# Optimization experiments

Measured on AMD Instinct MI355X. Metric: run time of the kernel, lower is better.

Reference implementation:

```python
import jax, jax.numpy as jnp
import numpy as np

N_NODES = 100000
N_EDGES = 1600000
IN_CH = 128
HID = 128
EMBED = 256
NUM_GRAPHS = 128


def setup_inputs() -> dict:
    key = jax.random.key(0)
    ks = jax.random.split(key, 12)
    x = jax.random.normal(ks[0], (N_NODES, IN_CH), dtype=jnp.float32)
    edge_index = jax.random.randint(ks[1], (2, N_EDGES), 0, N_NODES, dtype=jnp.int64)
    batch = jnp.sort(jax.random.randint(ks[2], (N_NODES,), 0, NUM_GRAPHS, dtype=jnp.int64))
    s = 0.05
    # conv1 MLP: Linear(in_ch,128) -> ReLU -> Linear(128,128)
    W11 = jax.random.normal(ks[3], (IN_CH, HID), dtype=jnp.float32) * s
    b11 = jnp.zeros((HID,), dtype=jnp.float32)
    W12 = jax.random.normal(ks[4], (HID, HID), dtype=jnp.float32) * s
    b12 = jnp.zeros((HID,), dtype=jnp.float32)
    # conv2 MLP: Linear(128,128) -> ReLU -> Linear(128,embed)
    W21 = jax.random.normal(ks[5], (HID, HID), dtype=jnp.float32) * s
    b21 = jnp.zeros((HID,), dtype=jnp.float32)
    W22 = jax.random.normal(ks[6], (HID, EMBED), dtype=jnp.float32) * s
    b22 = jnp.zeros((EMBED,), dtype=jnp.float32)
    gamma = jnp.ones((EMBED,), dtype=jnp.float32)
    beta = jnp.zeros((EMBED,), dtype=jnp.float32)
    return {"x": x, "edge_index": edge_index, "batch": batch,
            "W11": W11, "b11": b11, "W12": W12, "b12": b12,
            "W21": W21, "b21": b21, "W22": W22, "b22": b22,
            "gamma": gamma, "beta": beta}


def _gin_conv(x, src, dst, W_a, b_a, W_b, b_b):
    # GINConv with eps=0: MLP(x + sum_{j in N(i)} x_j)
    msgs = x[src]                                   # [E, d] gather
    agg = jax.ops.segment_sum(msgs, dst, num_segments=N_NODES)  # scatter-add
    h = x + agg
    h = jax.nn.relu(h @ W_a + b_a)
    return h @ W_b + b_b


def reference(x, edge_index, batch, W11, b11, W12, b12, W21, b21, W22, b22, gamma, beta):
    src, dst = edge_index[0], edge_index[1]
    h = jax.nn.relu(_gin_conv(x, src, dst, W11, b11, W12, b12))   # [N, 128]
    h = jax.nn.relu(_gin_conv(h, src, dst, W21, b21, W22, b22))   # [N, 256]
    # global_mean_pool over graphs
    sums = jax.ops.segment_sum(h, batch, num_segments=NUM_GRAPHS)           # [G, 256]
    counts = jax.ops.segment_sum(jnp.ones((N_NODES,), h.dtype), batch, num_segments=NUM_GRAPHS)
    pooled = sums / jnp.maximum(counts, 1.0)[:, None]
    # LayerNorm over last dim (eps=1e-5 as in torch)
    mu = jnp.mean(pooled, axis=-1, keepdims=True)
    var = jnp.var(pooled, axis=-1, keepdims=True)
    out = (pooled - mu) * jax.lax.rsqrt(var + 1e-5) * gamma + beta
    # Dropout in eval mode: identity
    return out
```

## Files before the change

kernel.cpp:

```cpp
#include <hip/hip_runtime.h>

#define GRAPHS 128
#define CHUNKC 4000

typedef _Float16 f16x8 __attribute__((ext_vector_type(8)));
typedef _Float16 f16x4 __attribute__((ext_vector_type(4)));
typedef _Float16 f16x2 __attribute__((ext_vector_type(2)));
typedef float f32x4 __attribute__((ext_vector_type(4)));

__device__ __forceinline__ void fmix_lo(float& a, int w) {
  asm("v_fma_mix_f32 %0, %1, 1.0, %0 op_sel:[0,0,0] op_sel_hi:[1,0,0]" : "+v"(a) : "v"(w));
}
__device__ __forceinline__ void fmix_hi(float& a, int w) {
  asm("v_fma_mix_f32 %0, %1, 1.0, %0 op_sel:[1,0,0] op_sel_hi:[1,0,0]" : "+v"(a) : "v"(w));
}

__global__ void k_prep(const int* __restrict__ dst, int* __restrict__ histG,
                       int e, int NB, int NW,
                       const float* __restrict__ x, _Float16* __restrict__ P0,
                       _Float16* __restrict__ P1, int n,
                       const float* __restrict__ W11, const float* __restrict__ W12,
                       const float* __restrict__ W21, const float* __restrict__ W22,
                       f16x8* __restrict__ f11, f16x8* __restrict__ f12,
                       f16x8* __restrict__ f21, f16x8* __restrict__ f22,
                       float* __restrict__ pool, int cvtb, int wpb, int poolb) {
  __shared__ int h[256];
  int b = blockIdx.x, t = threadIdx.x;
  if (b < NW) {
    h[t] = 0; __syncthreads();
    int lo = b * CHUNKC, hi = min(lo + CHUNKC, e);
    for (int i = lo + t; i < hi; i += 256) atomicAdd(&h[dst[i] >> 9], 1);
    __syncthreads();
    if (t < NB) histG[t * NW + b] = h[t];
    return;
  }
  b -= NW;
  if (b < cvtb) {
    int i = b * 256 + t;
    if (i < n * 32) {
      float4 v = ((const float4*)x)[i];
      f16x4 hh = { (_Float16)v.x, (_Float16)v.y, (_Float16)v.z, (_Float16)v.w };
      ((f16x4*)P0)[i] = hh;
    }
    return;
  }
  b -= cvtb;
  if (b < wpb) {
    int id = b * 256 + t;
    const float* W; f16x8* F; int C, cid, fshift;
    if (id < 2048)       { W = W11; F = f11; C = 128; cid = id;        fshift = 3; }
    else if (id < 4096)  { W = W12; F = f12; C = 128; cid = id - 2048; fshift = 3; }
    else if (id < 6144)  { W = W21; F = f21; C = 128; cid = id - 4096; fshift = 3; }
    else if (id < 10240) { W = W22; F = f22; C = 256; cid = id - 6144; fshift = 4; }
    else return;
    int lane = cid & 63;
    int rest = cid >> 6;
    int fc = rest & ((1 << fshift) - 1);
    int kk = rest >> fshift;
    int cout = fc * 16 + (lane & 15);
    int kb = kk * 32 + (lane >> 4) * 8;
    f16x8 v;
#pragma unroll
    for (int q = 0; q < 8; ++q) v[q] = (_Float16)W[(size_t)(kb + q) * C + cout];
    F[cid] = v;
    return;
  }
  b -= wpb;
  if (b < poolb) {
    int i = b * 256 + t;
    if (i < GRAPHS * 256) pool[i] = 0.f;
    return;
  }
  if (t < 128) P0[(size_t)n * 128 + t] = (_Float16)0.f;
  else P1[(size_t)n * 128 + (t - 128)] = (_Float16)0.f;
}

__global__ void k_scanA(const int* __restrict__ in, int* __restrict__ out,
                        int* __restrict__ bsum, int N) {
  __shared__ int s[256];
  int t = threadIdx.x, b = blockIdx.x;
  int base = b * 1024 + t * 4;
  int v[4]; int tot = 0;
#pragma unroll
  for (int j = 0; j < 4; ++j) { int i = base + j; v[j] = (i < N) ? in[i] : 0; tot += v[j]; }
  s[t] = tot; __syncthreads();
  for (int o = 1; o < 256; o <<= 1) {
    int x = (t >= o) ? s[t - o] : 0;
    __syncthreads(); s[t] += x; __syncthreads();
  }
  int run = s[t] - tot;
#pragma unroll
  for (int j = 0; j < 4; ++j) { int i = base + j; if (i < N) out[i] = run; run += v[j]; }
  if (t == 255) bsum[b] = s[255];
}

__global__ void k_scanB(int* bsum, int nb, const int* __restrict__ batch,
                        int* __restrict__ starts, int n) {
  __shared__ int s[256];
  int t = threadIdx.x;
  int v = (t < nb) ? bsum[t] : 0;
  s[t] = v; __syncthreads();
  for (int o = 1; o < 256; o <<= 1) {
    int x = (t >= o) ? s[t - o] : 0;
    __syncthreads(); s[t] += x; __syncthreads();
  }
  if (t < nb) bsum[t] = s[t] - v;
  if (t <= GRAPHS) {
    int lo = 0, hi = n;
    while (lo < hi) { int mid = (lo + hi) >> 1; if (batch[mid] < t) lo = mid + 1; else hi = mid; }
    starts[t] = lo;
  }
}

__global__ void k_part(const int* __restrict__ src, const int* __restrict__ dst,
                       const int* __restrict__ histG, const int* __restrict__ off,
                       const int* __restrict__ bsum,
                       int* __restrict__ part, int e, int NB, int NW) {
  __shared__ int hist[256], lbA[256], lbB[256], stmp[256];
  __shared__ int els[CHUNKC];
  int t = threadIdx.x, w = blockIdx.x;
  int hv = (t < NB) ? histG[t * NW + w] : 0;
  hist[t] = hv; stmp[t] = hv; __syncthreads();
  for (int o = 1; o < 256; o <<= 1) {
    int x = (t >= o) ? stmp[t - o] : 0;
    __syncthreads(); stmp[t] += x; __syncthreads();
  }
  lbA[t] = stmp[t] - hv; lbB[t] = stmp[t] - hv;
  __syncthreads();
  int lo = w * CHUNKC, hi = min(lo + CHUNKC, e);
  for (int i = lo + t; i < hi; i += 256) {
    int d = dst[i];
    int p = atomicAdd(&lbB[d >> 9], 1);
    els[p] = src[i] | ((d & 511) << 17);
  }
  __syncthreads();
  int ln = t & 63, wv = t >> 6;
  for (int b = wv; b < NB; b += 4) {
    int c = hist[b], lb = lbA[b];
    int idx = b * NW + w;
    long g = off[idx] + bsum[idx >> 10];
    for (int j = ln; j < c; j += 64) part[g + j] = els[lb + j];
  }
}

__global__ void k_csrb(const int* __restrict__ part, const int* __restrict__ off,
                       const int* __restrict__ bsum,
                       int* __restrict__ ptr, int* __restrict__ csr,
                       int e, int NB, int NW, int n) {
  __shared__ int nh[512], ncur[512], stmp[256];
  int t = threadIdx.x, b = blockIdx.x;
  int i0 = b * NW;
  int s0 = off[i0] + bsum[i0 >> 10];
  int e0 = e;
  if (b + 1 < NB) { int i1 = (b + 1) * NW; e0 = off[i1] + bsum[i1 >> 10]; }
  nh[t] = 0; nh[t + 256] = 0; __syncthreads();
  for (int i = s0 + t; i < e0; i += 256) atomicAdd(&nh[((unsigned)part[i]) >> 17], 1);
  __syncthreads();
  int v0 = nh[2 * t], v1 = nh[2 * t + 1];
  int ps = v0 + v1;
  stmp[t] = ps; __syncthreads();
  for (int o = 1; o < 256; o <<= 1) {
    int x = (t >= o) ? stmp[t - o] : 0;
    __syncthreads(); stmp[t] += x; __syncthreads();
  }
  int base = stmp[t] - ps;
  __syncthreads();
  nh[2 * t] = base;   nh[2 * t + 1] = base + v0;
  ncur[2 * t] = base; ncur[2 * t + 1] = base + v0;
  __syncthreads();
#pragma unroll
  for (int q = 0; q < 2; ++q) {
    int vv = t + q * 256;
    int node = (b << 9) + vv;
    if (node <= n) ptr[node] = s0 + nh[vv];
  }
  for (int i = s0 + t; i < e0; i += 256) {
    int u = part[i];
    int p = atomicAdd(&ncur[((unsigned)u) >> 17], 1);
    csr[s0 + p] = u & 0x1FFFF;
  }
}

__global__ void k_agg_h(const _Float16* __restrict__ in, _Float16* __restrict__ out,
                        const int* __restrict__ ptr, const int* __restrict__ csr, int n) {
  int gid = blockIdx.x * 256 + threadIdx.x;
  int node = gid >> 6, lane = gid & 63;
  if (node >= n) return;
  const f16x8* inp = (const f16x8*)in;
  int cb = lane & 15, rg = lane >> 4;
  f16x8 self = inp[(size_t)node * 16 + cb];
  float acc[8];
#pragma unroll
  for (int c = 0; c < 8; ++c) acc[c] = (rg == 0) ? (float)self[c] : 0.f;
  int s = ptr[node], deg = ptr[node + 1] - s;
  union W { f16x8 v; int i[4]; };
  for (int seg = 0; seg < deg; seg += 64) {
    int my = (seg + lane < deg) ? csr[s + seg + lane] : n;
    int segn = min(deg - seg, 64);
    for (int b2 = 0; b2 < segn; b2 += 32) {
      int jj[8]; W w[8];
#pragma unroll
      for (int u = 0; u < 8; ++u) jj[u] = __shfl(my, b2 + u * 4 + rg);
#pragma unroll
      for (int u = 0; u < 8; ++u) w[u].v = inp[(size_t)jj[u] * 16 + cb];
#pragma unroll
      for (int u = 0; u < 8; ++u)
#pragma unroll
        for (int p = 0; p < 4; ++p) {
          fmix_lo(acc[2 * p], w[u].i[p]);
          fmix_hi(acc[2 * p + 1], w[u].i[p]);
        }
    }
  }
#pragma unroll
  for (int c = 0; c < 8; ++c) {
    acc[c] += __shfl_xor(acc[c], 16);
    acc[c] += __shfl_xor(acc[c], 32);
  }
  if (rg == 0) {
    f16x8 r;
#pragma unroll
    for (int c = 0; c < 8; ++c) r[c] = (_Float16)acc[c];
    ((f16x8*)out)[(size_t)node * 16 + cb] = r;
  }
}

__device__ __forceinline__ f16x8 xpose(f32x4 aE, f32x4 aO, int rg) {
  union U2 { _Float16 h[2]; int i; };
  union U8 { int i[4]; f16x8 v; };
  U2 e01, e23, o01, o23;
  e01.h[0] = (_Float16)aE[0]; e01.h[1] = (_Float16)aE[1];
  e23.h[0] = (_Float16)aE[2]; e23.h[1] = (_Float16)aE[3];
  o01.h[0] = (_Float16)aO[0]; o01.h[1] = (_Float16)aO[1];
  o23.h[0] = (_Float16)aO[2]; o23.h[1] = (_Float16)aO[3];
  int e01x1 = __shfl_xor(e01.i, 16), e01x2 = __shfl_xor(e01.i, 32), e01x3 = __shfl_xor(e01.i, 48);
  int e23x1 = __shfl_xor(e23.i, 16), e23x2 = __shfl_xor(e23.i, 32), e23x3 = __shfl_xor(e23.i, 48);
  int o01x1 = __shfl_xor(o01.i, 16), o01x2 = __shfl_xor(o01.i, 32), o01x3 = __shfl_xor(o01.i, 48);
  int o23x1 = __shfl_xor(o23.i, 16), o23x2 = __shfl_xor(o23.i, 32), o23x3 = __shfl_xor(o23.i, 48);
  U8 r;
  r.i[0] = rg == 0 ? e01.i : rg == 1 ? e01x3 : rg == 2 ? o01x2 : o01x1;
  r.i[1] = rg == 0 ? e23.i : rg == 1 ? e23x3 : rg == 2 ? o23x2 : o23x1;
  r.i[2] = rg == 0 ? e01x1 : rg == 1 ? e01x2 : rg == 2 ? o01x3 : o01.i;
  r.i[3] = rg == 0 ? e23x1 : rg == 1 ? e23x2 : rg == 2 ? o23x3 : o23.i;
  return r.v;
}

__launch_bounds__(256, 3)
__global__ void k_mlp128(const _Float16* __restrict__ in, const f16x8* __restrict__ wfA,
                         const float* __restrict__ bA, const f16x8* __restrict__ wfB,
                         const float* __restrict__ bB, _Float16* __restrict__ out, int n) {
  __shared__ f16x8 wf[2048];
  int t = threadIdx.x;
  int r0 = blockIdx.x * 128;
  int lane = t & 63, w = t >> 6;
  int l16 = lane & 15, rg = lane >> 4;
  int rw = w * 32;
  const f16x8* inp = (const f16x8*)in;
#pragma unroll
  for (int i = 0; i < 8; ++i) wf[t + i * 256] = wfA[t + i * 256];
  int ra0 = r0 + rw + l16;      if (ra0 > n) ra0 = n;
  int ra1 = r0 + rw + 16 + l16; if (ra1 > n) ra1 = n;
  f16x8 xf[2][4];
#pragma unroll
  for (int kk = 0; kk < 4; ++kk) {
    xf[0][kk] = inp[(size_t)ra0 * 16 + kk * 4 + rg];
    xf[1][kk] = inp[(size_t)ra1 * 16 + kk * 4 + rg];
  }
  __syncthreads();
  f32x4 acc[2][8];
#pragma unroll
  for (int rs = 0; rs < 2; ++rs)
#pragma unroll
    for (int fc = 0; fc < 8; ++fc) acc[rs][fc] = (f32x4){0.f, 0.f, 0.f, 0.f};
#pragma unroll
  for (int kk = 0; kk < 4; ++kk)
#pragma unroll
    for (int fc = 0; fc < 8; ++fc) {
      f16x8 a = wf[(kk * 8 + fc) * 64 + lane];
      acc[0][fc] = __builtin_amdgcn_mfma_f32_16x16x32_f16(a, xf[0][kk], acc[0][fc], 0, 0, 0);
      acc[1][fc] = __builtin_amdgcn_mfma_f32_16x16x32_f16(a, xf[1][kk], acc[1][fc], 0, 0, 0);
    }
  f16x8 hf[2][4];
#pragma unroll
  for (int fc = 0; fc < 8; ++fc) {
    float4 bv = *(const float4*)(bA + fc * 16 + rg * 4);
#pragma unroll
    for (int rs = 0; rs < 2; ++rs) {
      acc[rs][fc][0] = fmaxf(acc[rs][fc][0] + bv.x, 0.f);
      acc[rs][fc][1] = fmaxf(acc[rs][fc][1] + bv.y, 0.f);
      acc[rs][fc][2] = fmaxf(acc[rs][fc][2] + bv.z, 0.f);
      acc[rs][fc][3] = fmaxf(acc[rs][fc][3] + bv.w, 0.f);
    }
  }
#pragma unroll
  for (int rs = 0; rs < 2; ++rs)
#pragma unroll
    for (int kk = 0; kk < 4; ++kk)
      hf[rs][kk] = xpose(acc[rs][2 * kk], acc[rs][2 * kk + 1], rg);
  __syncthreads();
#pragma unroll
  for (int i = 0; i < 8; ++i) wf[t + i * 256] = wfB[t + i * 256];
  __syncthreads();
#pragma unroll
  for (int rs = 0; rs < 2; ++rs)
#pragma unroll
    for (int fc = 0; fc < 8; ++fc) acc[rs][fc] = (f32x4){0.f, 0.f, 0.f, 0.f};
#pragma unroll
  for (int kk = 0; kk < 4; ++kk)
#pragma unroll
    for (int fc = 0; fc < 8; ++fc) {
      f16x8 b = wf[(kk * 8 + fc) * 64 + lane];
      acc[0][fc] = __builtin_amdgcn_mfma_f32_16x16x32_f16(b, hf[0][kk], acc[0][fc], 0, 0, 0);
      acc[1][fc] = __builtin_amdgcn_mfma_f32_16x16x32_f16(b, hf[1][kk], acc[1][fc], 0, 0, 0);
    }
#pragma unroll
  for (int fc = 0; fc < 8; ++fc) {
    float4 bv = *(const float4*)(bB + fc * 16 + rg * 4);
#pragma unroll
    for (int rs = 0; rs < 2; ++rs) {
      acc[rs][fc][0] = fmaxf(acc[rs][fc][0] + bv.x, 0.f);
      acc[rs][fc][1] = fmaxf(acc[rs][fc][1] + bv.y, 0.f);
      acc[rs][fc][2] = fmaxf(acc[rs][fc][2] + bv.z, 0.f);
      acc[rs][fc][3] = fmaxf(acc[rs][fc][3] + bv.w, 0.f);
    }
  }
  f16x8* outp = (f16x8*)out;
#pragma unroll
  for (int rs = 0; rs < 2; ++rs) {
    int row = r0 + rw + rs * 16 + l16;
#pragma unroll
    for (int kk = 0; kk < 4; ++kk) {
      f16x8 o = xpose(acc[rs][2 * kk], acc[rs][2 * kk + 1], rg);
      if (row < n) outp[(size_t)row * 16 + kk * 4 + rg] = o;
    }
  }
}

__launch_bounds__(256, 3)
__global__ void k_mlp_pool(const _Float16* __restrict__ in, const f16x8* __restrict__ wfA,
                           const float* __restrict__ bA, const f16x8* __restrict__ wfB,
                           const float* __restrict__ bB, const int* __restrict__ batch,
                           float* __restrict__ pool, float* __restrict__ scratch, int n) {
  __shared__ f16x8 wf[2048];
  __shared__ float pool_l[8 * 128 * 4];
  int t = threadIdx.x;
  int h = blockIdx.x & 1;
  int r0 = (blockIdx.x >> 1) * 128;
  int lane = t & 63, w = t >> 6;
  int l16 = lane & 15, rg = lane >> 4;
  int rw = w * 32;
  const f16x8* inp = (const f16x8*)in;
#pragma unroll
  for (int j = 0; j < 16; ++j) pool_l[j * 256 + t] = 0.f;
#pragma unroll
  for (int i = 0; i < 8; ++i) wf[t + i * 256] = wfA[t + i * 256];
  int ra0 = r0 + rw + l16;      if (ra0 > n) ra0 = n;
  int ra1 = r0 + rw + 16 + l16; if (ra1 > n) ra1 = n;
  f16x8 xf[2][4];
#pragma unroll
  for (int kk = 0; kk < 4; ++kk) {
    xf[0][kk] = inp[(size_t)ra0 * 16 + kk * 4 + rg];
    xf[1][kk] = inp[(size_t)ra1 * 16 + kk * 4 + rg];
  }
  int g0 = batch[r0];
  int rloc = rw + rg * 4;
  int g4[2][4];
#pragma unroll
  for (int fr = 0; fr < 2; ++fr)
#pragma unroll
    for (int j = 0; j < 4; ++j) {
      int row = r0 + rloc + fr * 16 + j;
      g4[fr][j] = (row < n) ? batch[row] : -1;
    }
  __syncthreads();
  f32x4 acc[2][8];
#pragma unroll
  for (int rs = 0; rs < 2; ++rs)
#pragma unroll
    for (int fc = 0; fc < 8; ++fc) acc[rs][fc] = (f32x4){0.f, 0.f, 0.f, 0.f};
#pragma unroll
  for (int kk = 0; kk < 4; ++kk)
#pragma unroll
    for (int fc = 0; fc < 8; ++fc) {
      f16x8 a = wf[(kk * 8 + fc) * 64 + lane];
      acc[0][fc] = __builtin_amdgcn_mfma_f32_16x16x32_f16(a, xf[0][kk], acc[0][fc], 0, 0, 0);
      acc[1][fc] = __builtin_amdgcn_mfma_f32_16x16x32_f16(a, xf[1][kk], acc[1][fc], 0, 0, 0);
    }
  f16x8 hf[2][4];
#pragma unroll
  for (int fc = 0; fc < 8; ++fc) {
    float4 bv = *(const float4*)(bA + fc * 16 + rg * 4);
#pragma unroll
    for (int rs = 0; rs < 2; ++rs) {
      acc[rs][fc][0] = fmaxf(acc[rs][fc][0] + bv.x, 0.f);
      acc[rs][fc][1] = fmaxf(acc[rs][fc][1] + bv.y, 0.f);
      acc[rs][fc][2] = fmaxf(acc[rs][fc][2] + bv.z, 0.f);
      acc[rs][fc][3] = fmaxf(acc[rs][fc][3] + bv.w, 0.f);
    }
  }
#pragma unroll
  for (int rs = 0; rs < 2; ++rs)
#pragma unroll
    for (int kk = 0; kk < 4; ++kk)
      hf[rs][kk] = xpose(acc[rs][2 * kk], acc[rs][2 * kk + 1], rg);
  __syncthreads();
#pragma unroll
  for (int i = 0; i < 8; ++i) {
    int id = t + i * 256;
    int lj = id & 63, fcl = (id >> 6) & 7, kk = id >> 9;
    wf[id] = wfB[(kk * 16 + h * 8 + fcl) * 64 + lj];
  }
  __syncthreads();
#pragma unroll
  for (int rs = 0; rs < 2; ++rs)
#pragma unroll
    for (int fc = 0; fc < 8; ++fc) acc[rs][fc] = (f32x4){0.f, 0.f, 0.f, 0.f};
#pragma unroll
  for (int kk = 0; kk < 4; ++kk)
#pragma unroll
    for (int fc = 0; fc < 8; ++fc) {
      f16x8 b = wf[(kk * 8 + fc) * 64 + lane];
      acc[0][fc] = __builtin_amdgcn_mfma_f32_16x16x32_f16(hf[0][kk], b, acc[0][fc], 0, 0, 0);
      acc[1][fc] = __builtin_amdgcn_mfma_f32_16x16x32_f16(hf[1][kk], b, acc[1][fc], 0, 0, 0);
    }
#pragma unroll
  for (int fc = 0; fc < 8; ++fc) {
    int col128 = fc * 16 + l16;
    float bv = bB[h * 128 + col128];
#pragma unroll
    for (int fr = 0; fr < 2; ++fr) {
      f32x4 a = acc[fr][fc];
      float run = fmaxf(a[0] + bv, 0.f);
#pragma unroll
      for (int j = 1; j < 4; ++j) {
        float v = fmaxf(a[j] + bv, 0.f);
        if (g4[fr][j] == g4[fr][j - 1]) run += v;
        else {
          int g = g4[fr][j - 1];
          if (g >= 0) {
            int d = g - g0;
            if (d >= 0 && d < 8) atomicAdd(&pool_l[(d * 128 + col128) * 4 + rg], run);
            else atomicAdd(&pool[g * 256 + h * 128 + col128], run);
          }
          run = v;
        }
      }
      int g = g4[fr][3];
      if (g >= 0) {
        int d = g - g0;
        if (d >= 0 && d < 8) atomicAdd(&pool_l[(d * 128 + col128) * 4 + rg], run);
        else atomicAdd(&pool[g * 256 + h * 128 + col128], run);
      }
    }
  }
  __syncthreads();
  float* sb = scratch + (size_t)blockIdx.x * 1024;
#pragma unroll
  for (int j = 0; j < 4; ++j) {
    int idx = j * 256 + t;
    float4 v4 = *(const float4*)&pool_l[idx * 4];
    sb[idx] = (v4.x + v4.y) + (v4.z + v4.w);
  }
}

__global__ void k_final(const float* __restrict__ scratch, const float* __restrict__ pool,
                        const int* __restrict__ starts, const int* __restrict__ batch,
                        const float* __restrict__ gamma, const float* __restrict__ beta,
                        float* __restrict__ out) {
  __shared__ float2 red[256];
  int g = blockIdx.x, ch = threadIdx.x;
  int h = ch >> 7, c = ch & 127;
  int s0 = starts[g], s1 = starts[g + 1];
  float p = pool[g * 256 + ch];
  if (s1 > s0) {
    int t0 = s0 >> 7, t1 = (s1 - 1) >> 7;
    for (int tile = t0; tile <= t1; ++tile) {
      int d = g - batch[tile << 7];
      if (d >= 0 && d < 8)
        p += scratch[(size_t)((tile << 1) | h) * 1024 + d * 128 + c];
    }
  }
  int cnt = s1 - s0;
  p /= fmaxf((float)cnt, 1.f);
  red[ch] = make_float2(p, p * p);
  __syncthreads();
  for (int off = 128; off > 0; off >>= 1) {
    if (ch < off) { red[ch].x += red[ch + off].x; red[ch].y += red[ch + off].y; }
    __syncthreads();
  }
  float mu = red[0].x * (1.f / 256.f);
  float var = red[0].y * (1.f / 256.f) - mu * mu;
  out[g * 256 + ch] = (p - mu) * rsqrtf(var + 1e-5f) * gamma[ch] + beta[ch];
}

extern "C" void kernel_launch(void* const* d_in, const int* in_sizes, int n_in,
                              void* d_out, int out_size, void* d_ws, size_t ws_size,
                              hipStream_t stream) {
  const float* x     = (const float*)d_in[0];
  const int*   ei    = (const int*)d_in[1];
  const int*   batch = (const int*)d_in[2];
  const float* W11 = (const float*)d_in[3];  const float* b11 = (const float*)d_in[4];
  const float* W12 = (const float*)d_in[5];  const float* b12 = (const float*)d_in[6];
  const float* W21 = (const float*)d_in[7];  const float* b21 = (const float*)d_in[8];
  const float* W22 = (const float*)d_in[9];  const float* b22 = (const float*)d_in[10];
  const float* gamma = (const float*)d_in[11];
  const float* beta  = (const float*)d_in[12];
  float* out = (float*)d_out;

  int n = in_sizes[0] / 128;
  int e = in_sizes[1] / 2;
  const int* src = ei;
  const int* dstv = ei + e;

  int NB = (n + 511) >> 9;
  int NW = (e + CHUNKC - 1) / CHUNKC;
  int NS = NB * NW;
  int mb = (n + 127) / 128;

  char* ws = (char*)d_ws;
  auto alloc = [&](size_t bytes) { char* p = ws; ws += (bytes + 15) & ~(size_t)15; return p; };
  _Float16* P0 = (_Float16*)alloc((size_t)(n + 1) * 128 * 2);
  _Float16* P1 = (_Float16*)alloc((size_t)(n + 1) * 128 * 2);
  float* pool  = (float*)alloc((size_t)GRAPHS * 256 * 4);
  float* scratch = (float*)alloc((size_t)mb * 2 * 1024 * 4);
  int* ptr     = (int*)alloc((size_t)(n + 1) * 4);
  int* csr     = (int*)alloc((size_t)e * 4);
  int* part    = (int*)alloc((size_t)e * 4);
  int* histG   = (int*)alloc((size_t)NS * 4);
  int* off     = (int*)alloc((size_t)NS * 4);
  int* bsum    = (int*)alloc(256 * 4);
  int* starts  = (int*)alloc((GRAPHS + 1) * 4);
  f16x8* f11 = (f16x8*)alloc(2048 * 16);
  f16x8* f12 = (f16x8*)alloc(2048 * 16);
  f16x8* f21 = (f16x8*)alloc(2048 * 16);
  f16x8* f22 = (f16x8*)alloc(4096 * 16);

  int cvtb = (n * 32 + 255) / 256;
  int wpb = 40;
  int poolb = (GRAPHS * 256 + 255) / 256;
  int prepb = NW + cvtb + wpb + poolb + 1;

  int nbk = (NS + 1023) / 1024;
  k_prep <<<prepb, 256, 0, stream>>>(dstv, histG, e, NB, NW, x, P0, P1, n,
                                     W11, W12, W21, W22, f11, f12, f21, f22,
                                     pool, cvtb, wpb, poolb);
  k_scanA<<<nbk, 256, 0, stream>>>(histG, off, bsum, NS);
  k_scanB<<<1, 256, 0, stream>>>(bsum, nbk, batch, starts, n);
  k_part <<<NW, 256, 0, stream>>>(src, dstv, histG, off, bsum, part, e, NB, NW);
  k_csrb <<<NB, 256, 0, stream>>>(part, off, bsum, ptr, csr, e, NB, NW, n);

  int ab = (n * 64 + 255) / 256;

  k_agg_h<<<ab, 256, 0, stream>>>(P0, P1, ptr, csr, n);
  k_mlp128<<<mb, 256, 0, stream>>>(P1, f11, b11, f12, b12, P0, n);
  k_agg_h<<<ab, 256, 0, stream>>>(P0, P1, ptr, csr, n);
  k_mlp_pool<<<mb * 2, 256, 0, stream>>>(P1, f21, b21, f22, b22, batch, pool, scratch, n);
  k_final<<<GRAPHS, 256, 0, stream>>>(scratch, pool, starts, batch, gamma, beta, out);
}
```

Before: 282.7 us.

## Make MLP kernels persistent with resident weights and prefetched next tile

Both MLP kernels become persistent grids of 512 blocks that loop over row tiles. Both weight matrices are loaded into shared memory once per block instead of per tile, and the next tile's input is prefetched into registers while the current one is computed. This cuts repeated weight staging and mid-kernel barriers, and lets input loads overlap MFMA work. In exchange it doubles shared memory, lowers the occupancy target to 2, and adds per-tile pool_l clearing plus barriers in the pooling kernel.

```diff
diff --git a/kernel.cpp b/kernel.cpp
--- a/kernel.cpp
+++ b/kernel.cpp
@@ -245,107 +245,132 @@
   return r.v;
 }
 
-__launch_bounds__(256, 3)
+__launch_bounds__(256, 2)
 __global__ void k_mlp128(const _Float16* __restrict__ in, const f16x8* __restrict__ wfA,
                          const float* __restrict__ bA, const f16x8* __restrict__ wfB,
-                         const float* __restrict__ bB, _Float16* __restrict__ out, int n) {
-  __shared__ f16x8 wf[2048];
+                         const float* __restrict__ bB, _Float16* __restrict__ out,
+                         int n, int mb) {
+  __shared__ f16x8 wa[2048];
+  __shared__ f16x8 wb[2048];
   int t = threadIdx.x;
-  int r0 = blockIdx.x * 128;
   int lane = t & 63, w = t >> 6;
   int l16 = lane & 15, rg = lane >> 4;
   int rw = w * 32;
   const f16x8* inp = (const f16x8*)in;
-#pragma unroll
-  for (int i = 0; i < 8; ++i) wf[t + i * 256] = wfA[t + i * 256];
-  int ra0 = r0 + rw + l16;      if (ra0 > n) ra0 = n;
-  int ra1 = r0 + rw + 16 + l16; if (ra1 > n) ra1 = n;
+  f16x8* outp = (f16x8*)out;
+#pragma unroll
+  for (int i = 0; i < 8; ++i) {
+    wa[t + i * 256] = wfA[t + i * 256];
+    wb[t + i * 256] = wfB[t + i * 256];
+  }
+  __syncthreads();
+  int tile = blockIdx.x;
   f16x8 xf[2][4];
-#pragma unroll
-  for (int kk = 0; kk < 4; ++kk) {
-    xf[0][kk] = inp[(size_t)ra0 * 16 + kk * 4 + rg];
-    xf[1][kk] = inp[(size_t)ra1 * 16 + kk * 4 + rg];
-  }
-  __syncthreads();
-  f32x4 acc[2][8];
-#pragma unroll
-  for (int rs = 0; rs < 2; ++rs)
-#pragma unroll
-    for (int fc = 0; fc < 8; ++fc) acc[rs][fc] = (f32x4){0.f, 0.f, 0.f, 0.f};
-#pragma unroll
-  for (int kk = 0; kk < 4; ++kk)
+  {
+    int r0 = tile * 128;
+    int ra0 = r0 + rw + l16;      if (ra0 > n) ra0 = n;
+    int ra1 = r0 + rw + 16 + l16; if (ra1 > n) ra1 = n;
+#pragma unroll
+    for (int kk = 0; kk < 4; ++kk) {
+      xf[0][kk] = inp[(size_t)ra0 * 16 + kk * 4 + rg];
+      xf[1][kk] = inp[(size_t)ra1 * 16 + kk * 4 + rg];
+    }
+  }
+  for (; tile < mb; tile += 512) {
+    f16x8 xn[2][4];
+    {
+      int nt = tile + 512;
+      int r0n = (nt < mb ? nt : tile) * 128;
+      int ra0 = r0n + rw + l16;      if (ra0 > n) ra0 = n;
+      int ra1 = r0n + rw + 16 + l16; if (ra1 > n) ra1 = n;
+#pragma unroll
+      for (int kk = 0; kk < 4; ++kk) {
+        xn[0][kk] = inp[(size_t)ra0 * 16 + kk * 4 + rg];
+        xn[1][kk] = inp[(size_t)ra1 * 16 + kk * 4 + rg];
+      }
+    }
+    int r0 = tile * 128;
+    f32x4 acc[2][8];
+#pragma unroll
+    for (int rs = 0; rs < 2; ++rs)
+#pragma unroll
+      for (int fc = 0; fc < 8; ++fc) acc[rs][fc] = (f32x4){0.f, 0.f, 0.f, 0.f};
+#pragma unroll
+    for (int kk = 0; kk < 4; ++kk)
+#pragma unroll
+      for (int fc = 0; fc < 8; ++fc) {
+        f16x8 a = wa[(kk * 8 + fc) * 64 + lane];
+        acc[0][fc] = __builtin_amdgcn_mfma_f32_16x16x32_f16(a, xf[0][kk], acc[0][fc], 0, 0, 0);
+        acc[1][fc] = __builtin_amdgcn_mfma_f32_16x16x32_f16(a, xf[1][kk], acc[1][fc], 0, 0, 0);
+      }
+    f16x8 hf[2][4];
 #pragma unroll
     for (int fc = 0; fc < 8; ++fc) {
-      f16x8 a = wf[(kk * 8 + fc) * 64 + lane];
-      acc[0][fc] = __builtin_amdgcn_mfma_f32_16x16x32_f16(a, xf[0][kk], acc[0][fc], 0, 0, 0);
-      acc[1][fc] = __builtin_amdgcn_mfma_f32_16x16x32_f16(a, xf[1][kk], acc[1][fc], 0, 0, 0);
-    }
-  f16x8 hf[2][4];
-#pragma unroll
-  for (int fc = 0; fc < 8; ++fc) {
-    float4 bv = *(const float4*)(bA + fc * 16 + rg * 4);
+      float4 bv = *(const float4*)(bA + fc * 16 + rg * 4);
+#pragma unroll
+      for (int rs = 0; rs < 2; ++rs) {
+        acc[rs][fc][0] = fmaxf(acc[rs][fc][0] + bv.x, 0.f);
+        acc[rs][fc][1] = fmaxf(acc[rs][fc][1] + bv.y, 0.f);
+        acc[rs][fc][2] = fmaxf(acc[rs][fc][2] + bv.z, 0.f);
+        acc[rs][fc][3] = fmaxf(acc[rs][fc][3] + bv.w, 0.f);
+      }
+    }
+#pragma unroll
+    for (int rs = 0; rs < 2; ++rs)
+#pragma unroll
+      for (int kk = 0; kk < 4; ++kk)
+        hf[rs][kk] = xpose(acc[rs][2 * kk], acc[rs][2 * kk + 1], rg);
+#pragma unroll
+    for (int rs = 0; rs < 2; ++rs)
+#pragma unroll
+      for (int fc = 0; fc < 8; ++fc) acc[rs][fc] = (f32x4){0.f, 0.f, 0.f, 0.f};
+#pragma unroll
+    for (int kk = 0; kk < 4; ++kk)
+#pragma unroll
+      for (int fc = 0; fc < 8; ++fc) {
+        f16x8 b = wb[(kk * 8 + fc) * 64 + lane];
+        acc[0][fc] = __builtin_amdgcn_mfma_f32_16x16x32_f16(b, hf[0][kk], acc[0][fc], 0, 0, 0);
+        acc[1][fc] = __builtin_amdgcn_mfma_f32_16x16x32_f16(b, hf[1][kk], acc[1][fc], 0, 0, 0);
+      }
+#pragma unroll
+    for (int fc = 0; fc < 8; ++fc) {
+      float4 bv = *(const float4*)(bB + fc * 16 + rg * 4);
+#pragma unroll
+      for (int rs = 0; rs < 2; ++rs) {
+        acc[rs][fc][0] = fmaxf(acc[rs][fc][0] + bv.x, 0.f);
+        acc[rs][fc][1] = fmaxf(acc[rs][fc][1] + bv.y, 0.f);
+        acc[rs][fc][2] = fmaxf(acc[rs][fc][2] + bv.z, 0.f);
+        acc[rs][fc][3] = fmaxf(acc[rs][fc][3] + bv.w, 0.f);
+      }
+    }
 #pragma unroll
     for (int rs = 0; rs < 2; ++rs) {
-      acc[rs][fc][0] = fmaxf(acc[rs][fc][0] + bv.x, 0.f);
-      acc[rs][fc][1] = fmaxf(acc[rs][fc][1] + bv.y, 0.f);
-      acc[rs][fc][2] = fmaxf(acc[rs][fc][2] + bv.z, 0.f);
-      acc[rs][fc][3] = fmaxf(acc[rs][fc][3] + bv.w, 0.f);
-    }
-  }
-#pragma unroll
-  for (int rs = 0; rs < 2; ++rs)
-#pragma unroll
-    for (int kk = 0; kk < 4; ++kk)
-      hf[rs][kk] = xpose(acc[rs][2 * kk], acc[rs][2 * kk + 1], rg);
-  __syncthreads();
-#pragma unroll
-  for (int i = 0; i < 8; ++i) wf[t + i * 256] = wfB[t + i * 256];
-  __syncthreads();
-#pragma unroll
-  for (int rs = 0; rs < 2; ++rs)
-#pragma unroll
-    for (int fc = 0; fc < 8; ++fc) acc[rs][fc] = (f32x4){0.f, 0.f, 0.f, 0.f};
-#pragma unroll
-  for (int kk = 0; kk < 4; ++kk)
-#pragma unroll
-    for (int fc = 0; fc < 8; ++fc) {
-      f16x8 b = wf[(kk * 8 + fc) * 64 + lane];
-      acc[0][fc] = __builtin_amdgcn_mfma_f32_16x16x32_f16(b, hf[0][kk], acc[0][fc], 0, 0, 0);
-      acc[1][fc] = __builtin_amdgcn_mfma_f32_16x16x32_f16(b, hf[1][kk], acc[1][fc], 0, 0, 0);
-    }
-#pragma unroll
-  for (int fc = 0; fc < 8; ++fc) {
-    float4 bv = *(const float4*)(bB + fc * 16 + rg * 4);
-#pragma unroll
-    for (int rs = 0; rs < 2; ++rs) {
-      acc[rs][fc][0] = fmaxf(acc[rs][fc][0] + bv.x, 0.f);
-      acc[rs][fc][1] = fmaxf(acc[rs][fc][1] + bv.y, 0.f);
-      acc[rs][fc][2] = fmaxf(acc[rs][fc][2] + bv.z, 0.f);
-      acc[rs][fc][3] = fmaxf(acc[rs][fc][3] + bv.w, 0.f);
-    }
-  }
-  f16x8* outp = (f16x8*)out;
-#pragma unroll
-  for (int rs = 0; rs < 2; ++rs) {
-    int row = r0 + rw + rs * 16 + l16;
-#pragma unroll
-    for (int kk = 0; kk < 4; ++kk) {
-      f16x8 o = xpose(acc[rs][2 * kk], acc[rs][2 * kk + 1], rg);
-      if (row < n) outp[(size_t)row * 16 + kk * 4 + rg] = o;
-    }
-  }
-}
-
-__launch_bounds__(256, 3)
+      int row = r0 + rw + rs * 16 + l16;
+#pragma unroll
+      for (int kk = 0; kk < 4; ++kk) {
+        f16x8 o = xpose(acc[rs][2 * kk], acc[rs][2 * kk + 1], rg);
+        if (row < n) outp[(size_t)row * 16 + kk * 4 + rg] = o;
+      }
+    }
+#pragma unroll
+    for (int rs = 0; rs < 2; ++rs)
+#pragma unroll
+      for (int kk = 0; kk < 4; ++kk) xf[rs][kk] = xn[rs][kk];
+  }
+}
+
+__launch_bounds__(256, 2)
 __global__ void k_mlp_pool(const _Float16* __restrict__ in, const f16x8* __restrict__ wfA,
                            const float* __restrict__ bA, const f16x8* __restrict__ wfB,
                            const float* __restrict__ bB, const int* __restrict__ batch,
-                           float* __restrict__ pool, float* __restrict__ scratch, int n) {
-  __shared__ f16x8 wf[2048];
+                           float* __restrict__ pool, float* __restrict__ scratch,
+                           int n, int mb) {
+  __shared__ f16x8 wa[2048];
+  __shared__ f16x8 wb[2048];
   __shared__ float pool_l[8 * 128 * 4];
   int t = threadIdx.x;
   int h = blockIdx.x & 1;
-  int r0 = (blockIdx.x >> 1) * 128;
+  int slot = blockIdx.x >> 1;
   int lane = t & 63, w = t >> 6;
   int l16 = lane & 15, rg = lane >> 4;
   int rw = w * 32;
@@ -353,113 +378,135 @@
 #pragma unroll
   for (int j = 0; j < 16; ++j) pool_l[j * 256 + t] = 0.f;
 #pragma unroll
-  for (int i = 0; i < 8; ++i) wf[t + i * 256] = wfA[t + i * 256];
-  int ra0 = r0 + rw + l16;      if (ra0 > n) ra0 = n;
-  int ra1 = r0 + rw + 16 + l16; if (ra1 > n) ra1 = n;
-  f16x8 xf[2][4];
-#pragma unroll
-  for (int kk = 0; kk < 4; ++kk) {
-    xf[0][kk] = inp[(size_t)ra0 * 16 + kk * 4 + rg];
-    xf[1][kk] = inp[(size_t)ra1 * 16 + kk * 4 + rg];
-  }
-  int g0 = batch[r0];
-  int rloc = rw + rg * 4;
-  int g4[2][4];
-#pragma unroll
-  for (int fr = 0; fr < 2; ++fr)
-#pragma unroll
-    for (int j = 0; j < 4; ++j) {
-      int row = r0 + rloc + fr * 16 + j;
-      g4[fr][j] = (row < n) ? batch[row] : -1;
-    }
-  __syncthreads();
-  f32x4 acc[2][8];
-#pragma unroll
-  for (int rs = 0; rs < 2; ++rs)
-#pragma unroll
-    for (int fc = 0; fc < 8; ++fc) acc[rs][fc] = (f32x4){0.f, 0.f, 0.f, 0.f};
-#pragma unroll
-  for (int kk = 0; kk < 4; ++kk)
-#pragma unroll
-    for (int fc = 0; fc < 8; ++fc) {
-      f16x8 a = wf[(kk * 8 + fc) * 64 + lane];
-      acc[0][fc] = __builtin_amdgcn_mfma_f32_16x16x32_f16(a, xf[0][kk], acc[0][fc], 0, 0, 0);
-      acc[1][fc] = __builtin_amdgcn_mfma_f32_16x16x32_f16(a, xf[1][kk], acc[1][fc], 0, 0, 0);
-    }
-  f16x8 hf[2][4];
-#pragma unroll
-  for (int fc = 0; fc < 8; ++fc) {
-    float4 bv = *(const float4*)(bA + fc * 16 + rg * 4);
-#pragma unroll
-    for (int rs = 0; rs < 2; ++rs) {
-      acc[rs][fc][0] = fmaxf(acc[rs][fc][0] + bv.x, 0.f);
-      acc[rs][fc][1] = fmaxf(acc[rs][fc][1] + bv.y, 0.f);
-      acc[rs][fc][2] = fmaxf(acc[rs][fc][2] + bv.z, 0.f);
-      acc[rs][fc][3] = fmaxf(acc[rs][fc][3] + bv.w, 0.f);
-    }
-  }
-#pragma unroll
-  for (int rs = 0; rs < 2; ++rs)
-#pragma unroll
-    for (int kk = 0; kk < 4; ++kk)
-      hf[rs][kk] = xpose(acc[rs][2 * kk], acc[rs][2 * kk + 1], rg);
-  __syncthreads();
-#pragma unroll
   for (int i = 0; i < 8; ++i) {
     int id = t + i * 256;
     int lj = id & 63, fcl = (id >> 6) & 7, kk = id >> 9;
-    wf[id] = wfB[(kk * 16 + h * 8 + fcl) * 64 + lj];
-  }
-  __syncthreads();
-#pragma unroll
-  for (int rs = 0; rs < 2; ++rs)
-#pragma unroll
-    for (int fc = 0; fc < 8; ++fc) acc[rs][fc] = (f32x4){0.f, 0.f, 0.f, 0.f};
-#pragma unroll
-  for (int kk = 0; kk < 4; ++kk)
+    wa[id] = wfA[id];
+    wb[id] = wfB[(kk * 16 + h * 8 + fcl) * 64 + lj];
+  }
+  __syncthreads();
+  int tile = slot;
+  f16x8 xf[2][4];
+  {
+    int r0 = tile * 128;
+    int ra0 = r0 + rw + l16;      if (ra0 > n) ra0 = n;
+    int ra1 = r0 + rw + 16 + l16; if (ra1 > n) ra1 = n;
+#pragma unroll
+    for (int kk = 0; kk < 4; ++kk) {
+      xf[0][kk] = inp[(size_t)ra0 * 16 + kk * 4 + rg];
+      xf[1][kk] = inp[(size_t)ra1 * 16 + kk * 4 + rg];
+    }
+  }
+  for (; tile < mb; tile += 256) {
+    f16x8 xn[2][4];
+    {
+      int nt = tile + 256;
+      int r0n = (nt < mb ? nt : tile) * 128;
+      int ra0 = r0n + rw + l16;      if (ra0 > n) ra0 = n;
+      int ra1 = r0n + rw + 16 + l16; if (ra1 > n) ra1 = n;
+#pragma unroll
+      for (int kk = 0; kk < 4; ++kk) {
+        xn[0][kk] = inp[(size_t)ra0 * 16 + kk * 4 + rg];
+        xn[1][kk] = inp[(size_t)ra1 * 16 + kk * 4 + rg];
+      }
+    }
+    int r0 = tile * 128;
+    int g0 = batch[r0];
+    int rloc = rw + rg * 4;
+    int g4[2][4];
+#pragma unroll
+    for (int fr = 0; fr < 2; ++fr)
+#pragma unroll
+      for (int j = 0; j < 4; ++j) {
+        int row = r0 + rloc + fr * 16 + j;
+        g4[fr][j] = (row < n) ? batch[row] : -1;
+      }
+    f32x4 acc[2][8];
+#pragma unroll
+    for (int rs = 0; rs < 2; ++rs)
+#pragma unroll
+      for (int fc = 0; fc < 8; ++fc) acc[rs][fc] = (f32x4){0.f, 0.f, 0.f, 0.f};
+#pragma unroll
+    for (int kk = 0; kk < 4; ++kk)
+#pragma unroll
+      for (int fc = 0; fc < 8; ++fc) {
+        f16x8 a = wa[(kk * 8 + fc) * 64 + lane];
+        acc[0][fc] = __builtin_amdgcn_mfma_f32_16x16x32_f16(a, xf[0][kk], acc[0][fc], 0, 0, 0);
+        acc[1][fc] = __builtin_amdgcn_mfma_f32_16x16x32_f16(a, xf[1][kk], acc[1][fc], 0, 0, 0);
+      }
+    f16x8 hf[2][4];
 #pragma unroll
     for (int fc = 0; fc < 8; ++fc) {
-      f16x8 b = wf[(kk * 8 + fc) * 64 + lane];
-      acc[0][fc] = __builtin_amdgcn_mfma_f32_16x16x32_f16(hf[0][kk], b, acc[0][fc], 0, 0, 0);
-      acc[1][fc] = __builtin_amdgcn_mfma_f32_16x16x32_f16(hf[1][kk], b, acc[1][fc], 0, 0, 0);
-    }
-#pragma unroll
-  for (int fc = 0; fc < 8; ++fc) {
-    int col128 = fc * 16 + l16;
-    float bv = bB[h * 128 + col128];
-#pragma unroll
-    for (int fr = 0; fr < 2; ++fr) {
-      f32x4 a = acc[fr][fc];
-      float run = fmaxf(a[0] + bv, 0.f);
-#pragma unroll
-      for (int j = 1; j < 4; ++j) {
-        float v = fmaxf(a[j] + bv, 0.f);
-        if (g4[fr][j] == g4[fr][j - 1]) run += v;
-        else {
-          int g = g4[fr][j - 1];
-          if (g >= 0) {
-            int d = g - g0;
-            if (d >= 0 && d < 8) atomicAdd(&pool_l[(d * 128 + col128) * 4 + rg], run);
-            else atomicAdd(&pool[g * 256 + h * 128 + col128], run);
+      float4 bv = *(const float4*)(bA + fc * 16 + rg * 4);
+#pragma unroll
+      for (int rs = 0; rs < 2; ++rs) {
+        acc[rs][fc][0] = fmaxf(acc[rs][fc][0] + bv.x, 0.f);
+        acc[rs][fc][1] = fmaxf(acc[rs][fc][1] + bv.y, 0.f);
+        acc[rs][fc][2] = fmaxf(acc[rs][fc][2] + bv.z, 0.f);
+        acc[rs][fc][3] = fmaxf(acc[rs][fc][3] + bv.w, 0.f);
+      }
+    }
+#pragma unroll
+    for (int rs = 0; rs < 2; ++rs)
+#pragma unroll
+      for (int kk = 0; kk < 4; ++kk)
+        hf[rs][kk] = xpose(acc[rs][2 * kk], acc[rs][2 * kk + 1], rg);
+#pragma unroll
+    for (int rs = 0; rs < 2; ++rs)
+#pragma unroll
+      for (int fc = 0; fc < 8; ++fc) acc[rs][fc] = (f32x4){0.f, 0.f, 0.f, 0.f};
+#pragma unroll
+    for (int kk = 0; kk < 4; ++kk)
+#pragma unroll
+      for (int fc = 0; fc < 8; ++fc) {
+        f16x8 b = wb[(kk * 8 + fc) * 64 + lane];
+        acc[0][fc] = __builtin_amdgcn_mfma_f32_16x16x32_f16(hf[0][kk], b, acc[0][fc], 0, 0, 0);
+        acc[1][fc] = __builtin_amdgcn_mfma_f32_16x16x32_f16(hf[1][kk], b, acc[1][fc], 0, 0, 0);
+      }
+#pragma unroll
+    for (int fc = 0; fc < 8; ++fc) {
+      int col128 = fc * 16 + l16;
+      float bv = bB[h * 128 + col128];
+#pragma unroll
+      for (int fr = 0; fr < 2; ++fr) {
+        f32x4 a = acc[fr][fc];
+        float run = fmaxf(a[0] + bv, 0.f);
+#pragma unroll
+        for (int j = 1; j < 4; ++j) {
+          float v = fmaxf(a[j] + bv, 0.f);
+          if (g4[fr][j] == g4[fr][j - 1]) run += v;
+          else {
+            int g = g4[fr][j - 1];
+            if (g >= 0) {
+              int d = g - g0;
+              if (d >= 0 && d < 8) atomicAdd(&pool_l[(d * 128 + col128) * 4 + rg], run);
+              else atomicAdd(&pool[g * 256 + h * 128 + col128], run);
+            }
+            run = v;
           }
-          run = v;
         }
-      }
-      int g = g4[fr][3];
-      if (g >= 0) {
-        int d = g - g0;
-        if (d >= 0 && d < 8) atomicAdd(&pool_l[(d * 128 + col128) * 4 + rg], run);
-        else atomicAdd(&pool[g * 256 + h * 128 + col128], run);
-      }
-    }
-  }
-  __syncthreads();
-  float* sb = scratch + (size_t)blockIdx.x * 1024;
-#pragma unroll
-  for (int j = 0; j < 4; ++j) {
-    int idx = j * 256 + t;
-    float4 v4 = *(const float4*)&pool_l[idx * 4];
-    sb[idx] = (v4.x + v4.y) + (v4.z + v4.w);
+        int g = g4[fr][3];
+        if (g >= 0) {
+          int d = g - g0;
+          if (d >= 0 && d < 8) atomicAdd(&pool_l[(d * 128 + col128) * 4 + rg], run);
+          else atomicAdd(&pool[g * 256 + h * 128 + col128], run);
+        }
+      }
+    }
+    __syncthreads();
+    float* sb = scratch + (size_t)((tile << 1) | h) * 1024;
+#pragma unroll
+    for (int j = 0; j < 4; ++j) {
+      int idx = j * 256 + t;
+      float4 v4 = *(const float4*)&pool_l[idx * 4];
+      sb[idx] = (v4.x + v4.y) + (v4.z + v4.w);
+      *(float4*)&pool_l[idx * 4] = make_float4(0.f, 0.f, 0.f, 0.f);
+    }
+    __syncthreads();
+#pragma unroll
+    for (int rs = 0; rs < 2; ++rs)
+#pragma unroll
+      for (int kk = 0; kk < 4; ++kk) xf[rs][kk] = xn[rs][kk];
   }
 }
 
@@ -552,8 +599,8 @@
   int ab = (n * 64 + 255) / 256;
 
   k_agg_h<<<ab, 256, 0, stream>>>(P0, P1, ptr, csr, n);
-  k_mlp128<<<mb, 256, 0, stream>>>(P1, f11, b11, f12, b12, P0, n);
+  k_mlp128<<<512, 256, 0, stream>>>(P1, f11, b11, f12, b12, P0, n, mb);
   k_agg_h<<<ab, 256, 0, stream>>>(P0, P1, ptr, csr, n);
-  k_mlp_pool<<<mb * 2, 256, 0, stream>>>(P1, f21, b21, f22, b22, batch, pool, scratch, n);
+  k_mlp_pool<<<512, 256, 0, stream>>>(P1, f21, b21, f22, b22, batch, pool, scratch, n, mb);
   k_final<<<GRAPHS, 256, 0, stream>>>(scratch, pool, starts, batch, gamma, beta, out);
 }
```

Result: slower. 332.7 us (+17.7%).
